# Kernel optimization log

Measured on AMD Instinct MI355X. Metric: run time of the kernel, lower is better.

The kernel has to match this reference:

```python
import jax, jax.numpy as jnp
import numpy as np

# RadixAttention EXTEND forward: queries over newly-extended tokens attend to
# (a) the full cached prefix KV (non-causal) and (b) the extend-token KV (causal),
# equivalent to attention over concat([prefix, extend]) with a shifted causal mask.

SCALING = 0.08838834764831845  # 1/sqrt(128)


def setup_inputs() -> dict:
    key = jax.random.key(0)
    k1, k2, k3, k4, k5 = jax.random.split(key, 5)
    B, E, P, H, Hk, D = 4, 512, 1536, 32, 8, 128
    return {
        "q": jax.random.normal(k1, (B, E, H, D), dtype=jnp.float32),
        "k": jax.random.normal(k2, (B, E, Hk, D), dtype=jnp.float32),
        "v": jax.random.normal(k3, (B, E, Hk, D), dtype=jnp.float32),
        "k_cache": jax.random.normal(k4, (B, P, Hk, D), dtype=jnp.float32),
        "v_cache": jax.random.normal(k5, (B, P, Hk, D), dtype=jnp.float32),
    }


def reference(q, k, v, k_cache, v_cache):
    B, E, H, D = q.shape
    Hk = k.shape[2]
    P = k_cache.shape[1]
    g = H // Hk  # GQA group size
    S = P + E

    k_all = jnp.concatenate([k_cache, k], axis=1)  # [B, S, Hk, D]
    v_all = jnp.concatenate([v_cache, v], axis=1)  # [B, S, Hk, D]

    qg = q.reshape(B, E, Hk, g, D)
    # scores: [B, Hk, g, E, S]
    scores = jnp.einsum("bekgd,bskd->bkges", qg, k_all) * SCALING

    # key j visible to extend-query e iff j <= P + e (prefix fully visible, extend causal)
    visible = jnp.arange(S)[None, :] <= (P + jnp.arange(E))[:, None]  # [E, S]
    scores = jnp.where(visible[None, None, None, :, :], scores, jnp.float32(-1e30))

    p = jax.nn.softmax(scores, axis=-1)
    o = jnp.einsum("bkges,bskd->bekgd", p, v_all).reshape(B, E, H, D)
    # module returns flat [num_tokens, H*D]
    return o.reshape(B * E, H * D)
```

## Files before the change

### kernel.cpp

```cpp
#include <hip/hip_runtime.h>
#include <hip/hip_bf16.h>
#include <stdint.h>
#include <stddef.h>


#define B_ 4
#define E_ 512
#define P_ 1536
#define H_ 32
#define HK_ 8
#define D_ 128
#define G_ 4
#define S_ 2048

#define BLOCK_E 32
#define NT 64
#define TPITCH 72
#define KVSTRIDE (HK_ * D_)
#define NTHREADS 512
#define M_FIX 12.0f
#define TILE_SHORTS 8192

typedef __attribute__((ext_vector_type(8))) short short8v;
typedef __attribute__((ext_vector_type(4))) float floatx4;

__device__ __forceinline__ short2 f2bf2(float a, float b) {
  __hip_bfloat162 h = __float22bfloat162_rn(float2{a, b});
  return *(short2*)&h;
}
__device__ __forceinline__ short f2bf(float f) {
  union { float f; uint32_t u; } x; x.f = f;
  uint32_t r = x.u + 0x7FFFu + ((x.u >> 16) & 1u);
  return (short)(r >> 16);
}
__device__ __forceinline__ short8v cvt8(const float4 a, const float4 b) {
  short2 p0 = f2bf2(a.x, a.y), p1 = f2bf2(a.z, a.w);
  short2 p2 = f2bf2(b.x, b.y), p3 = f2bf2(b.z, b.w);
  short8v f;
  f[0] = p0.x; f[1] = p0.y; f[2] = p1.x; f[3] = p1.y;
  f[4] = p2.x; f[5] = p2.y; f[6] = p3.x; f[7] = p3.y;
  return f;
}

__global__ __launch_bounds__(256)
void prep_kv(const float* __restrict__ kc, const float* __restrict__ ke,
             const float* __restrict__ vc, const float* __restrict__ ve,
             short* __restrict__ kb, short* __restrict__ vt) {
  __shared__ short TT[D_ * TPITCH];
  const int bid = blockIdx.x;
  const int tid = threadIdx.x;
  if (bid < 4096) {
    const int cid = bid * 256 + tid;
    const int cl  = cid & 15;
    const int j   = (cid >> 4) & (S_ - 1);
    const int kh  = (cid >> 15) & 7;
    const int b   = cid >> 18;
    const float* src = (j < P_)
        ? (kc + (((size_t)b * P_ + j) * HK_ + kh) * D_ + cl * 8)
        : (ke + (((size_t)b * E_ + (j - P_)) * HK_ + kh) * D_ + cl * 8);
    const float4 x0 = *(const float4*)src;
    const float4 x1 = *(const float4*)(src + 4);
    const int t = j >> 6, key = j & 63;
    const int cs = ((cl & 7) ^ (key & 7)) | (cl & 8);
    *(short8v*)&kb[(((size_t)(b * 8 + kh) * 32 + t)) * TILE_SHORTS + key * 128 + cs * 8] =
        cvt8(x0, x1);
  } else {
    const int b2 = bid - 4096;
    const int j0 = (b2 & 31) * 64;
    const int kh = (b2 >> 5) & 7;
    const int b  = b2 >> 8;
#pragma unroll
    for (int it = 0; it < 8; ++it) {
      const int linear = it * 256 + tid;
      const int key = linear >> 5;
      const int dof = (linear & 31) * 4;
      const int j = j0 + key;
      const float* src = (j < P_)
          ? (vc + (((size_t)b * P_ + j) * HK_ + kh) * D_ + dof)
          : (ve + (((size_t)b * E_ + (j - P_)) * HK_ + kh) * D_ + dof);
      const float4 x = *(const float4*)src;
      short2 a = f2bf2(x.x, x.y), c = f2bf2(x.z, x.w);
      TT[(dof + 0) * TPITCH + key] = a.x;
      TT[(dof + 1) * TPITCH + key] = a.y;
      TT[(dof + 2) * TPITCH + key] = c.x;
      TT[(dof + 3) * TPITCH + key] = c.y;
    }
    __syncthreads();
#pragma unroll
    for (int it = 0; it < 4; ++it) {
      const int linear = it * 256 + tid;
      const int d  = linear >> 3;
      const int ck = linear & 7;
      const int cks = ck ^ (d & 7);
      *(short8v*)&vt[(((size_t)(b * 8 + kh) * 32 + (j0 >> 6))) * TILE_SHORTS + d * 64 + cks * 8] =
          *(const short8v*)&TT[d * TPITCH + ck * 8];
    }
  }
}

__global__ __launch_bounds__(NTHREADS, 4)
void radix_attn(const float* __restrict__ q,
                const short* __restrict__ kb,
                const short* __restrict__ vt,
                float* __restrict__ out) {
  __shared__ short KT[2][NT * D_];
  __shared__ short VTs[2][D_ * NT];
  __shared__ short PW[8][1024];

  const int flat = blockIdx.x;
  const int kh   = flat & 7;
  const int b    = (flat >> 3) & 3;
  const int e0   = (flat >> 5) * BLOCK_E;
  const int tid  = threadIdx.x;
  const int wave = tid >> 6;
  const int lane = tid & 63;
  const int quad = lane >> 4;
  const int l16  = lane & 15;
  const int gi   = wave & 3;
  const int rb   = wave >> 2;
  const int h    = kh * G_ + gi;

  short8v qf[4];
  {
    const int e = e0 + rb * 16 + l16;
    const float* qp = q + (((size_t)b * E_ + e) * H_ + h) * D_ + quad * 8;
#pragma unroll
    for (int kcc = 0; kcc < 4; ++kcc)
      qf[kcc] = cvt8(*(const float4*)(qp + kcc * 32), *(const float4*)(qp + kcc * 32 + 4));
  }

  short8v ones8;
#pragma unroll
  for (int i = 0; i < 8; ++i) ones8[i] = (l16 == 0) ? (short)0x3F80 : (short)0;

  floatx4 oacc[8];
#pragma unroll
  for (int dt = 0; dt < 8; ++dt) oacc[dt] = (floatx4){0.f, 0.f, 0.f, 0.f};
  floatx4 acc_l = (floatx4){0.f, 0.f, 0.f, 0.f};

  const short* kbt = kb + (size_t)(b * 8 + kh) * 32 * TILE_SHORTS;
  const short* vtt = vt + (size_t)(b * 8 + kh) * 32 * TILE_SHORTS;

  const int slimit = P_ + e0 + BLOCK_E;
  const int ntiles = (slimit + NT - 1) / NT;
  const float sc = 0.08838834764831845f * 1.44269504088896340f;

  const int qlim = P_ + e0 + rb * 16 + l16;
  const int pb   = l16 * 64;
  const int swz  = l16 & 7;

  auto dma = [&](int t, int buf) {
    const char* kg = (const char*)kbt + (size_t)t * 16384 + wave * 2048 + lane * 16;
    const char* vg = (const char*)vtt + (size_t)t * 16384 + wave * 2048 + lane * 16;
    short* kl = &KT[buf][wave * 1024];
    short* vl = &VTs[buf][wave * 1024];
#pragma unroll
    for (int g = 0; g < 2; ++g) {
      __builtin_amdgcn_global_load_lds(
          (const __attribute__((address_space(1))) void*)(kg + g * 1024),
          (__attribute__((address_space(3))) void*)(kl + g * 512), 16, 0, 0);
      __builtin_amdgcn_global_load_lds(
          (const __attribute__((address_space(1))) void*)(vg + g * 1024),
          (__attribute__((address_space(3))) void*)(vl + g * 512), 16, 0, 0);
    }
  };

  auto tile = [&](int t, int cur) {
    const int kt0 = t * NT;

    __syncthreads();
    if (t + 1 < ntiles) dma(t + 1, cur ^ 1);

    floatx4 sfr[4];
    __builtin_amdgcn_s_setprio(1);
#pragma unroll
    for (int nc = 0; nc < 4; ++nc) {
      short8v kf[4];
#pragma unroll
      for (int kcc = 0; kcc < 4; ++kcc) {
        const int cl = kcc * 4 + quad;
        const int cs = ((cl & 7) ^ swz) | (cl & 8);
        kf[kcc] = *(const short8v*)&KT[cur][(nc * 16 + l16) * D_ + cs * 8];
      }
      floatx4 acc = (floatx4){0.f, 0.f, 0.f, 0.f};
#pragma unroll
      for (int kcc = 0; kcc < 4; ++kcc)
        acc = __builtin_amdgcn_mfma_f32_16x16x32_bf16(kf[kcc], qf[kcc], acc, 0, 0, 0);
      sfr[nc] = acc;
    }
    __builtin_amdgcn_s_setprio(0);

    short8v vfr[4];
#pragma unroll
    for (int dt = 0; dt < 4; ++dt) {
      const int cs = quad ^ swz;
      vfr[dt] = *(const short8v*)&VTs[cur][(dt * 16 + l16) * NT + cs * 8];
    }

    const bool need_mask = (kt0 + NT - 1 > P_ + e0 + rb * 16);
#pragma unroll
    for (int nc = 0; nc < 4; ++nc) {
      float p[4];
#pragma unroll
      for (int reg = 0; reg < 4; ++reg) {
        float pe = __builtin_amdgcn_exp2f(__builtin_fmaf(sfr[nc][reg], sc, -M_FIX));
        if (need_mask) {
          const int jkey = kt0 + nc * 16 + quad * 4 + reg;
          if (jkey > qlim) pe = 0.f;
        }
        p[reg] = pe;
      }
      const short2 a = f2bf2(p[0], p[1]), c = f2bf2(p[2], p[3]);
      short4 y; y.x = a.x; y.y = a.y; y.z = c.x; y.w = c.y;
      const int ch = (nc * 2 + (quad >> 1)) ^ swz;
      *(short4*)&PW[wave][pb + ch * 8 + (quad & 1) * 4] = y;
    }
    short8v pf[2];
#pragma unroll
    for (int kc = 0; kc < 2; ++kc)
      pf[kc] = *(const short8v*)&PW[wave][pb + ((kc * 4 + quad) ^ swz) * 8];

    __builtin_amdgcn_s_setprio(1);
#pragma unroll
    for (int kc = 0; kc < 2; ++kc) {
#pragma unroll
      for (int dt = 0; dt < 8; ++dt) {
        short8v vf;
        if (kc == 0 && dt < 4) {
          vf = vfr[dt];
        } else {
          const int cs = (kc * 4 + quad) ^ swz;
          vf = *(const short8v*)&VTs[cur][(dt * 16 + l16) * NT + cs * 8];
        }
        oacc[dt] = __builtin_amdgcn_mfma_f32_16x16x32_bf16(pf[kc], vf, oacc[dt], 0, 0, 0);
      }
      acc_l = __builtin_amdgcn_mfma_f32_16x16x32_bf16(pf[kc], ones8, acc_l, 0, 0, 0);
    }
    __builtin_amdgcn_s_setprio(0);
  };

  dma(0, 0);
  int t = 0;
  for (; t + 2 <= ntiles; t += 2) {
    tile(t, 0);
    tile(t + 1, 1);
  }
  if (t < ntiles) tile(t, 0);

  float inv[4];
#pragma unroll
  for (int reg = 0; reg < 4; ++reg) {
    const float l = __shfl(acc_l[reg], lane & 48, 64);
    inv[reg] = 1.0f / l;
  }
#pragma unroll
  for (int reg = 0; reg < 4; ++reg) {
    const int erow = e0 + rb * 16 + quad * 4 + reg;
    float* op = out + (size_t)(b * E_ + erow) * (H_ * D_) + h * D_ + l16;
#pragma unroll
    for (int dt = 0; dt < 8; ++dt)
      op[dt * 16] = oacc[dt][reg] * inv[reg];
  }
}

__global__ __launch_bounds__(1024, 4)
void radix_attn_fp32(const float* __restrict__ q,
                     const float* __restrict__ ke,
                     const float* __restrict__ ve,
                     const float* __restrict__ kc,
                     const float* __restrict__ vc,
                     float* __restrict__ out) {
  __shared__ short KT[NT * 136];
  __shared__ short VTs[D_ * TPITCH];
  __shared__ short PW[16][16 * 80];
  const int flat = blockIdx.x;
  const int kh = flat & 7, b = (flat >> 3) & 3, e0 = (flat >> 5) * 64;
  const int tid = threadIdx.x, wave = tid >> 6, lane = tid & 63;
  const int quad = lane >> 4, l16 = lane & 15;
  const int gi = wave & 3, rbw = wave >> 2, h = kh * G_ + gi;
  short8v qf[4];
  {
    const int e = e0 + rbw * 16 + l16;
    const float* qp = q + (((size_t)b * E_ + e) * H_ + h) * D_ + quad * 8;
#pragma unroll
    for (int kcc = 0; kcc < 4; ++kcc)
      qf[kcc] = cvt8(*(const float4*)(qp + kcc * 32), *(const float4*)(qp + kcc * 32 + 4));
  }
  short8v ones8;
#pragma unroll
  for (int i = 0; i < 8; ++i) ones8[i] = (l16 == 0) ? (short)0x3F80 : (short)0;
  floatx4 oacc[8];
#pragma unroll
  for (int d = 0; d < 8; ++d) oacc[d] = (floatx4){0.f, 0.f, 0.f, 0.f};
  floatx4 acc_l = (floatx4){0.f, 0.f, 0.f, 0.f};
  float mrow[4];
#pragma unroll
  for (int r = 0; r < 4; ++r) mrow[r] = -1e30f;
  const float* kcb = kc + (size_t)b * P_ * KVSTRIDE + (size_t)kh * D_;
  const float* keb = ke + (size_t)b * E_ * KVSTRIDE + (size_t)kh * D_;
  const float* vcb = vc + (size_t)b * P_ * KVSTRIDE + (size_t)kh * D_;
  const float* veb = ve + (size_t)b * E_ * KVSTRIDE + (size_t)kh * D_;
  const int ntiles = (P_ + e0 + 64) / NT;
  const float sc = 0.08838834764831845f * 1.44269504088896340f;
  for (int t = 0; t < ntiles; ++t) {
    const int kt0 = t * NT;
    __syncthreads();
#pragma unroll
    for (int it = 0; it < 2; ++it) {
      const int linear = it * 1024 + tid;
      const int key = linear >> 5, dof = (linear & 31) * 4;
      const int j = kt0 + key;
      const float* src = (j < P_) ? (kcb + (size_t)j * KVSTRIDE) : (keb + (size_t)(j - P_) * KVSTRIDE);
      const float4 x = *(const float4*)(src + dof);
      short2 a = f2bf2(x.x, x.y), c = f2bf2(x.z, x.w);
      short4 y; y.x = a.x; y.y = a.y; y.z = c.x; y.w = c.y;
      *(short4*)&KT[key * 136 + dof] = y;
    }
#pragma unroll
    for (int it = 0; it < 2; ++it) {
      const int linear = it * 1024 + tid;
      const int key = linear & 63, dg = (linear >> 6) * 4;
      const int j = kt0 + key;
      const float* src = (j < P_) ? (vcb + (size_t)j * KVSTRIDE) : (veb + (size_t)(j - P_) * KVSTRIDE);
      const float4 x = *(const float4*)(src + dg);
      short2 a = f2bf2(x.x, x.y), c = f2bf2(x.z, x.w);
      VTs[(dg + 0) * TPITCH + key] = a.x;
      VTs[(dg + 1) * TPITCH + key] = a.y;
      VTs[(dg + 2) * TPITCH + key] = c.x;
      VTs[(dg + 3) * TPITCH + key] = c.y;
    }
    __syncthreads();
    floatx4 sfr[4];
#pragma unroll
    for (int nc = 0; nc < 4; ++nc) {
      floatx4 acc = (floatx4){0.f, 0.f, 0.f, 0.f};
#pragma unroll
      for (int kcc = 0; kcc < 4; ++kcc) {
        const short8v bf = *(const short8v*)&KT[(nc * 16 + l16) * 136 + kcc * 32 + quad * 8];
        acc = __builtin_amdgcn_mfma_f32_16x16x32_bf16(qf[kcc], bf, acc, 0, 0, 0);
      }
      sfr[nc] = acc;
    }
    const bool need_mask = (kt0 + NT - 1 > P_ + e0 + rbw * 16);
#pragma unroll
    for (int nc = 0; nc < 4; ++nc)
#pragma unroll
      for (int reg = 0; reg < 4; ++reg) {
        float s = sfr[nc][reg] * sc;
        if (need_mask) {
          const int jkey = kt0 + nc * 16 + l16;
          const int erow = e0 + rbw * 16 + quad * 4 + reg;
          if (jkey > P_ + erow) s = -1e30f;
        }
        sfr[nc][reg] = s;
      }
    float mt[4];
#pragma unroll
    for (int reg = 0; reg < 4; ++reg)
      mt[reg] = fmaxf(fmaxf(sfr[0][reg], sfr[1][reg]), fmaxf(sfr[2][reg], sfr[3][reg]));
#pragma unroll
    for (int off = 1; off < 16; off <<= 1)
#pragma unroll
      for (int reg = 0; reg < 4; ++reg)
        mt[reg] = fmaxf(mt[reg], __shfl_xor(mt[reg], off, 64));
#pragma unroll
    for (int reg = 0; reg < 4; ++reg) {
      const float mnew = fmaxf(mrow[reg], mt[reg]);
      const float alpha = __builtin_amdgcn_exp2f(mrow[reg] - mnew);
      mrow[reg] = mnew;
      acc_l[reg] *= alpha;
#pragma unroll
      for (int d = 0; d < 8; ++d) oacc[d][reg] *= alpha;
    }
#pragma unroll
    for (int nc = 0; nc < 4; ++nc)
#pragma unroll
      for (int reg = 0; reg < 4; ++reg) {
        const float p = __builtin_amdgcn_exp2f(sfr[nc][reg] - mrow[reg]);
        PW[wave][(quad * 4 + reg) * 80 + nc * 16 + l16] = f2bf(p);
      }
    const short8v pf0 = *(const short8v*)&PW[wave][l16 * 80 + quad * 8];
    const short8v pf1 = *(const short8v*)&PW[wave][l16 * 80 + 32 + quad * 8];
#pragma unroll
    for (int d = 0; d < 8; ++d) {
      const short8v vf0 = *(const short8v*)&VTs[(d * 16 + l16) * TPITCH + quad * 8];
      const short8v vf1 = *(const short8v*)&VTs[(d * 16 + l16) * TPITCH + 32 + quad * 8];
      oacc[d] = __builtin_amdgcn_mfma_f32_16x16x32_bf16(pf0, vf0, oacc[d], 0, 0, 0);
      oacc[d] = __builtin_amdgcn_mfma_f32_16x16x32_bf16(pf1, vf1, oacc[d], 0, 0, 0);
    }
    acc_l = __builtin_amdgcn_mfma_f32_16x16x32_bf16(pf0, ones8, acc_l, 0, 0, 0);
    acc_l = __builtin_amdgcn_mfma_f32_16x16x32_bf16(pf1, ones8, acc_l, 0, 0, 0);
  }
  float inv[4];
#pragma unroll
  for (int reg = 0; reg < 4; ++reg)
    inv[reg] = 1.0f / __shfl(acc_l[reg], lane & 48, 64);
#pragma unroll
  for (int reg = 0; reg < 4; ++reg) {
    const int erow = e0 + rbw * 16 + quad * 4 + reg;
    float* op = out + (size_t)(b * E_ + erow) * (H_ * D_) + h * D_ + l16;
#pragma unroll
    for (int d = 0; d < 8; ++d)
      op[d * 16] = oacc[d][reg] * inv[reg];
  }
}

extern "C" void kernel_launch(void* const* d_in, const int* in_sizes, int n_in,
                              void* d_out, int out_size, void* d_ws, size_t ws_size,
                              hipStream_t stream) {
  const float* q  = (const float*)d_in[0];
  const float* ke = (const float*)d_in[1];
  const float* ve = (const float*)d_in[2];
  const float* kc = (const float*)d_in[3];
  const float* vc = (const float*)d_in[4];
  float* out = (float*)d_out;

  const size_t kv_shorts = (size_t)B_ * HK_ * S_ * D_;
  const size_t need = 2 * kv_shorts * sizeof(short);

  if (ws_size >= need) {
    short* kb = (short*)d_ws;
    short* vt = kb + kv_shorts;
    prep_kv<<<dim3(4096 + 1024), dim3(256), 0, stream>>>(kc, ke, vc, ve, kb, vt);
    const int nblk = (E_ / BLOCK_E) * HK_ * B_;
    radix_attn<<<dim3(nblk), dim3(NTHREADS), 0, stream>>>(q, kb, vt, out);
  } else {
    radix_attn_fp32<<<dim3(8 * 8 * 4), dim3(1024), 0, stream>>>(q, ke, ve, kc, vc, out);
  }
}
```

Baseline: 218.7 us.

## Keep P in registers via 16x16x16 MFMA and split V-transpose prep blocks

The attention kernel now computes P·V with the 16x16x16 bf16 MFMA, ordering operands so the exponentiated score fragment feeds the MFMA straight from registers. This removes the per-tile LDS round trip through the PW scratch buffer, and the row sum comes from an all-ones operand, so the final normalisation no longer needs a shuffle. Output is written as float4 rows. The V-transpose prep is split into twice as many half-tile blocks, each writing rows contiguously to LDS and gathering columns on read. In exchange, PV needs twice as many MFMA instructions, each on narrower fragments.

Result: slower. 231.0 us (+5.6%).

```diff
diff --git a/kernel.cpp b/kernel.cpp
--- a/kernel.cpp
+++ b/kernel.cpp
@@ -21,7 +21,17 @@
 #define M_FIX 12.0f
 #define TILE_SHORTS 8192
 
+#ifndef __has_builtin
+#define __has_builtin(x) 0
+#endif
+#if __has_builtin(__builtin_amdgcn_mfma_f32_16x16x16bf16_1k)
+#define HAVE_MFMA16 1
+#else
+#define HAVE_MFMA16 0
+#endif
+
 typedef __attribute__((ext_vector_type(8))) short short8v;
+typedef __attribute__((ext_vector_type(4))) short short4v;
 typedef __attribute__((ext_vector_type(4))) float floatx4;
 
 __device__ __forceinline__ short2 f2bf2(float a, float b) {
@@ -46,7 +56,7 @@
 void prep_kv(const float* __restrict__ kc, const float* __restrict__ ke,
              const float* __restrict__ vc, const float* __restrict__ ve,
              short* __restrict__ kb, short* __restrict__ vt) {
-  __shared__ short TT[D_ * TPITCH];
+  __shared__ short TK[32 * 132];
   const int bid = blockIdx.x;
   const int tid = threadIdx.x;
   if (bid < 4096) {
@@ -65,12 +75,14 @@
     *(short8v*)&kb[(((size_t)(b * 8 + kh) * 32 + t)) * TILE_SHORTS + key * 128 + cs * 8] =
         cvt8(x0, x1);
   } else {
-    const int b2 = bid - 4096;
-    const int j0 = (b2 & 31) * 64;
-    const int kh = (b2 >> 5) & 7;
-    const int b  = b2 >> 8;
-#pragma unroll
-    for (int it = 0; it < 8; ++it) {
+    const int b2   = bid - 4096;
+    const int half = b2 & 1;
+    const int tile = (b2 >> 1) & 31;
+    const int kh   = (b2 >> 6) & 7;
+    const int b    = b2 >> 9;
+    const int j0   = tile * 64 + half * 32;
+#pragma unroll
+    for (int it = 0; it < 4; ++it) {
       const int linear = it * 256 + tid;
       const int key = linear >> 5;
       const int dof = (linear & 31) * 4;
@@ -80,20 +92,22 @@
           : (ve + (((size_t)b * E_ + (j - P_)) * HK_ + kh) * D_ + dof);
       const float4 x = *(const float4*)src;
       short2 a = f2bf2(x.x, x.y), c = f2bf2(x.z, x.w);
-      TT[(dof + 0) * TPITCH + key] = a.x;
-      TT[(dof + 1) * TPITCH + key] = a.y;
-      TT[(dof + 2) * TPITCH + key] = c.x;
-      TT[(dof + 3) * TPITCH + key] = c.y;
+      short4 y; y.x = a.x; y.y = a.y; y.z = c.x; y.w = c.y;
+      *(short4*)&TK[key * 132 + dof] = y;
     }
     __syncthreads();
-#pragma unroll
-    for (int it = 0; it < 4; ++it) {
+    short* dst = vt + (((size_t)(b * 8 + kh) * 32 + tile)) * TILE_SHORTS;
+#pragma unroll
+    for (int it = 0; it < 2; ++it) {
       const int linear = it * 256 + tid;
-      const int d  = linear >> 3;
-      const int ck = linear & 7;
-      const int cks = ck ^ (d & 7);
-      *(short8v*)&vt[(((size_t)(b * 8 + kh) * 32 + (j0 >> 6))) * TILE_SHORTS + d * 64 + cks * 8] =
-          *(const short8v*)&TT[d * TPITCH + ck * 8];
+      const int d   = linear >> 2;
+      const int ckl = linear & 3;
+      const int ckg = half * 4 + ckl;
+      const int cks = ckg ^ (d & 7);
+      short8v v;
+#pragma unroll
+      for (int i = 0; i < 8; ++i) v[i] = TK[(ckl * 8 + i) * 132 + d];
+      *(short8v*)&dst[d * 64 + cks * 8] = v;
     }
   }
 }
@@ -105,7 +119,9 @@
                 float* __restrict__ out) {
   __shared__ short KT[2][NT * D_];
   __shared__ short VTs[2][D_ * NT];
+#if !HAVE_MFMA16
   __shared__ short PW[8][1024];
+#endif
 
   const int flat = blockIdx.x;
   const int kh   = flat & 7;
@@ -129,14 +145,20 @@
       qf[kcc] = cvt8(*(const float4*)(qp + kcc * 32), *(const float4*)(qp + kcc * 32 + 4));
   }
 
-  short8v ones8;
-#pragma unroll
-  for (int i = 0; i < 8; ++i) ones8[i] = (l16 == 0) ? (short)0x3F80 : (short)0;
-
   floatx4 oacc[8];
 #pragma unroll
   for (int dt = 0; dt < 8; ++dt) oacc[dt] = (floatx4){0.f, 0.f, 0.f, 0.f};
   floatx4 acc_l = (floatx4){0.f, 0.f, 0.f, 0.f};
+
+#if HAVE_MFMA16
+  short4v ones4;
+#pragma unroll
+  for (int i = 0; i < 4; ++i) ones4[i] = (short)0x3F80;
+#else
+  short8v ones8;
+#pragma unroll
+  for (int i = 0; i < 8; ++i) ones8[i] = (l16 == 0) ? (short)0x3F80 : (short)0;
+#endif
 
   const short* kbt = kb + (size_t)(b * 8 + kh) * 32 * TILE_SHORTS;
   const short* vtt = vt + (size_t)(b * 8 + kh) * 32 * TILE_SHORTS;
@@ -146,7 +168,6 @@
   const float sc = 0.08838834764831845f * 1.44269504088896340f;
 
   const int qlim = P_ + e0 + rb * 16 + l16;
-  const int pb   = l16 * 64;
   const int swz  = l16 & 7;
 
   auto dma = [&](int t, int buf) {
@@ -190,14 +211,16 @@
     }
     __builtin_amdgcn_s_setprio(0);
 
-    short8v vfr[4];
-#pragma unroll
-    for (int dt = 0; dt < 4; ++dt) {
-      const int cs = quad ^ swz;
-      vfr[dt] = *(const short8v*)&VTs[cur][(dt * 16 + l16) * NT + cs * 8];
-    }
-
     const bool need_mask = (kt0 + NT - 1 > P_ + e0 + rb * 16);
+
+#if HAVE_MFMA16
+    short4v vpre[4];
+#pragma unroll
+    for (int dt = 0; dt < 4; ++dt)
+      vpre[dt] = *(const short4v*)&VTs[cur][(dt * 16 + l16) * NT +
+                                           ((quad >> 1) ^ swz) * 8 + (quad & 1) * 4];
+
+    short4v pf[4];
 #pragma unroll
     for (int nc = 0; nc < 4; ++nc) {
       float p[4];
@@ -211,15 +234,56 @@
         p[reg] = pe;
       }
       const short2 a = f2bf2(p[0], p[1]), c = f2bf2(p[2], p[3]);
+      short4v y; y[0] = a.x; y[1] = a.y; y[2] = c.x; y[3] = c.y;
+      pf[nc] = y;
+    }
+
+    __builtin_amdgcn_s_setprio(1);
+#pragma unroll
+    for (int nc = 0; nc < 4; ++nc) {
+#pragma unroll
+      for (int dt = 0; dt < 8; ++dt) {
+        short4v vf;
+        if (nc == 0 && dt < 4) {
+          vf = vpre[dt];
+        } else {
+          const int cks = (nc * 2 + (quad >> 1)) ^ swz;
+          vf = *(const short4v*)&VTs[cur][(dt * 16 + l16) * NT + cks * 8 + (quad & 1) * 4];
+        }
+        oacc[dt] = __builtin_amdgcn_mfma_f32_16x16x16bf16_1k(vf, pf[nc], oacc[dt], 0, 0, 0);
+      }
+      acc_l = __builtin_amdgcn_mfma_f32_16x16x16bf16_1k(ones4, pf[nc], acc_l, 0, 0, 0);
+    }
+    __builtin_amdgcn_s_setprio(0);
+#else
+    short8v vfr[4];
+#pragma unroll
+    for (int dt = 0; dt < 4; ++dt) {
+      const int cs = quad ^ swz;
+      vfr[dt] = *(const short8v*)&VTs[cur][(dt * 16 + l16) * NT + cs * 8];
+    }
+    const int pb = l16 * 64;
+#pragma unroll
+    for (int nc = 0; nc < 4; ++nc) {
+      float p[4];
+#pragma unroll
+      for (int reg = 0; reg < 4; ++reg) {
+        float pe = __builtin_amdgcn_exp2f(__builtin_fmaf(sfr[nc][reg], sc, -M_FIX));
+        if (need_mask) {
+          const int jkey = kt0 + nc * 16 + quad * 4 + reg;
+          if (jkey > qlim) pe = 0.f;
+        }
+        p[reg] = pe;
+      }
+      const short2 a = f2bf2(p[0], p[1]), c = f2bf2(p[2], p[3]);
       short4 y; y.x = a.x; y.y = a.y; y.z = c.x; y.w = c.y;
       const int ch = (nc * 2 + (quad >> 1)) ^ swz;
       *(short4*)&PW[wave][pb + ch * 8 + (quad & 1) * 4] = y;
     }
-    short8v pf[2];
+    short8v pfx[2];
 #pragma unroll
     for (int kc = 0; kc < 2; ++kc)
-      pf[kc] = *(const short8v*)&PW[wave][pb + ((kc * 4 + quad) ^ swz) * 8];
-
+      pfx[kc] = *(const short8v*)&PW[wave][pb + ((kc * 4 + quad) ^ swz) * 8];
     __builtin_amdgcn_s_setprio(1);
 #pragma unroll
     for (int kc = 0; kc < 2; ++kc) {
@@ -232,11 +296,12 @@
           const int cs = (kc * 4 + quad) ^ swz;
           vf = *(const short8v*)&VTs[cur][(dt * 16 + l16) * NT + cs * 8];
         }
-        oacc[dt] = __builtin_amdgcn_mfma_f32_16x16x32_bf16(pf[kc], vf, oacc[dt], 0, 0, 0);
-      }
-      acc_l = __builtin_amdgcn_mfma_f32_16x16x32_bf16(pf[kc], ones8, acc_l, 0, 0, 0);
+        oacc[dt] = __builtin_amdgcn_mfma_f32_16x16x32_bf16(pfx[kc], vf, oacc[dt], 0, 0, 0);
+      }
+      acc_l = __builtin_amdgcn_mfma_f32_16x16x32_bf16(pfx[kc], ones8, acc_l, 0, 0, 0);
     }
     __builtin_amdgcn_s_setprio(0);
+#endif
   };
 
   dma(0, 0);
@@ -247,6 +312,18 @@
   }
   if (t < ntiles) tile(t, 0);
 
+#if HAVE_MFMA16
+  const float inv = 1.0f / acc_l[0];
+  const int erow = e0 + rb * 16 + l16;
+  float* op = out + (size_t)(b * E_ + erow) * (H_ * D_) + h * D_ + quad * 4;
+#pragma unroll
+  for (int dt = 0; dt < 8; ++dt) {
+    float4 v;
+    v.x = oacc[dt][0] * inv; v.y = oacc[dt][1] * inv;
+    v.z = oacc[dt][2] * inv; v.w = oacc[dt][3] * inv;
+    *(float4*)(op + dt * 16) = v;
+  }
+#else
   float inv[4];
 #pragma unroll
   for (int reg = 0; reg < 4; ++reg) {
@@ -261,6 +338,7 @@
     for (int dt = 0; dt < 8; ++dt)
       op[dt * 16] = oacc[dt][reg] * inv[reg];
   }
+#endif
 }
 
 __global__ __launch_bounds__(1024, 4)
@@ -421,7 +499,7 @@
   if (ws_size >= need) {
     short* kb = (short*)d_ws;
     short* vt = kb + kv_shorts;
-    prep_kv<<<dim3(4096 + 1024), dim3(256), 0, stream>>>(kc, ke, vc, ve, kb, vt);
+    prep_kv<<<dim3(4096 + 2048), dim3(256), 0, stream>>>(kc, ke, vc, ve, kb, vt);
     const int nblk = (E_ / BLOCK_E) * HK_ * B_;
     radix_attn<<<dim3(nblk), dim3(NTHREADS), 0, stream>>>(q, kb, vt, out);
   } else {
```
